# Kernel optimization log

Hardware: AMD Instinct MI355X
Metric: run time of the kernel (lower is better)

The kernel has to match this reference:

```python
import jax, jax.numpy as jnp
import numpy as np

BS, T, FIN, FOUT = 8, 1024, 512, 512
ALPHA = 0.1      # leaky relu slope
T_K = 3          # t_ksize (odd); temporal band radius = T_K // 2
S_K = 4          # s_ksize semantic topk
NEG_INF = -9e15


def setup_inputs() -> dict:
    key = jax.random.key(0)
    k1, k2, k3, k4 = jax.random.split(key, 4)
    # xavier-uniform-ish scales (gain 1.414)
    w_lim = 1.414 * np.sqrt(6.0 / (FIN + FOUT))
    a_lim = 1.414 * np.sqrt(6.0 / (2 * FOUT + 1))
    return {
        "x_a": jax.random.normal(k1, (BS, T, FIN), jnp.float32),
        "x_v": jax.random.normal(k2, (BS, T, FIN), jnp.float32),
        "W": jax.random.uniform(k3, (FIN, FOUT), jnp.float32, -w_lim, w_lim),
        "a": jax.random.uniform(k4, (2 * FOUT, 1), jnp.float32, -a_lim, a_lim),
    }


def _temporal_mask(t):
    # tem_adj[i,j] = 1 iff |i-j| <= T_K//2 and i, j on the same side of t-0.5
    idx = jnp.arange(2 * t)
    same_side = (idx[:, None] >= t) == (idx[None, :] >= t)
    band = jnp.abs(idx[:, None] - idx[None, :]) <= (T_K // 2)
    return band & same_side  # (2t, 2t) bool


def _semantic_block_mask(x, k):
    # x: (bs, t, d). Top-k neighbors by negative squared euclidean distance.
    inner = 2.0 * jnp.einsum("btd,bsd->bts", x, x)
    sq = jnp.sum(x * x, axis=-1, keepdims=True)  # (bs, t, 1)
    pd = -(sq - inner + jnp.swapaxes(sq, -1, -2))  # (bs, t, t)
    _, idx = jax.lax.top_k(pd, k)  # (bs, t, k)
    bs, t = x.shape[0], x.shape[1]
    b_ix = jnp.arange(bs)[:, None, None]
    r_ix = jnp.arange(t)[None, :, None]
    return jnp.zeros((bs, t, t), bool).at[b_ix, r_ix, idx].set(True)


def reference(x_a, x_v, W, a):
    bs, t, _ = x_a.shape
    h = jnp.concatenate([x_a, x_v], axis=1)          # (bs, 2t, FIN)
    Wh = h @ W                                        # (bs, 2t, FOUT)

    # additive GAT score: e = leakyrelu(Wh a1 + (Wh a2)^T)
    Wh1 = Wh @ a[:FOUT]                               # (bs, 2t, 1)
    Wh2 = Wh @ a[FOUT:]                               # (bs, 2t, 1)
    e = Wh1 + jnp.swapaxes(Wh2, -1, -2)               # (bs, 2t, 2t)
    e = jnp.where(e > 0, e, ALPHA * e)                # leaky relu

    # adjacency: temporal band + semantic topk within aa / vv blocks
    tem = _temporal_mask(t)                           # (2t, 2t)
    sem_aa = _semantic_block_mask(Wh[:, :t], S_K)     # (bs, t, t)
    sem_vv = _semantic_block_mask(Wh[:, t:], S_K)     # (bs, t, t)
    zb = jnp.zeros((bs, t, t), bool)
    sem = jnp.concatenate([
        jnp.concatenate([sem_aa, zb], axis=-1),
        jnp.concatenate([zb, sem_vv], axis=-1),
    ], axis=1)                                        # (bs, 2t, 2t)
    mask = tem[None] | sem

    attention = jax.nn.softmax(jnp.where(mask, e, NEG_INF), axis=-1)
    h_prime = jax.nn.elu(attention @ Wh)              # (bs, 2t, FOUT)
    return h_prime[:, :t], h_prime[:, t:]
```

## Files before the change

kernel.cpp:

```cpp
#include <hip/hip_runtime.h>
#include <math.h>

#define T_ 1024
#define BS_ 8
#define D_ 512
#define NROWS_ (BS_*2*T_)
#define ALPHA_ 0.1f

typedef _Float16 f16;
typedef _Float16 f16x8 __attribute__((ext_vector_type(8)));
typedef _Float16 f16x4 __attribute__((ext_vector_type(4)));
typedef _Float16 f16x2 __attribute__((ext_vector_type(2)));
typedef float f32x4 __attribute__((ext_vector_type(4)));

#define MFMA16(A,B,C) __builtin_amdgcn_mfma_f32_16x16x32_f16((A),(B),(C),0,0,0)

__device__ __forceinline__ void gl16(const void* g, void* l) {
    __builtin_amdgcn_global_load_lds(
        (const __attribute__((address_space(1))) unsigned int*)g,
        (__attribute__((address_space(3))) unsigned int*)l, 16, 0, 0);
}

#if __has_builtin(__builtin_amdgcn_fdot2)
__device__ __forceinline__ float fdot2p(f16x2 a, f16x2 b, float c) {
    return __builtin_amdgcn_fdot2(a, b, c, false);
}
#else
__device__ __forceinline__ float fdot2p(f16x2 a, f16x2 b, float c) {
    return fmaf((float)a[1], (float)b[1], fmaf((float)a[0], (float)b[0], c));
}
#endif

__device__ __forceinline__ float fdot8(const f16x8 a, const f16x8 b, float s) {
    #pragma unroll
    for (int q = 0; q < 4; ++q) {
        f16x2 aa, bb;
        aa[0] = a[2*q]; aa[1] = a[2*q+1];
        bb[0] = b[2*q]; bb[1] = b[2*q+1];
        s = fdot2p(aa, bb, s);
    }
    return s;
}

__device__ __forceinline__ unsigned sortable(float f) {
    unsigned u = __float_as_uint(f);
    return u ^ ((u & 0x80000000u) ? 0xFFFFFFFFu : 0x80000000u);
}
__device__ __forceinline__ unsigned pack_key(float s, int col) {
    return (sortable(s) & 0xFFFFFC00u) | (unsigned)(1023 - col);
}

#define INSK4(K, X) { \
    bool g3 = (X) > K[3], g2 = (X) > K[2], g1 = (X) > K[1], g0 = (X) > K[0]; \
    K[3] = g2 ? K[2] : (g3 ? (X) : K[3]); \
    K[2] = g1 ? K[1] : (g2 ? (X) : K[2]); \
    K[1] = g0 ? K[0] : (g1 ? (X) : K[1]); \
    K[0] = g0 ? (X) : K[0]; }

#define INSK8(K, X) { \
    bool h7=(X)>K[7],h6=(X)>K[6],h5=(X)>K[5],h4=(X)>K[4]; \
    bool h3=(X)>K[3],h2=(X)>K[2],h1=(X)>K[1],h0=(X)>K[0]; \
    K[7]=h6?K[6]:(h7?(X):K[7]); K[6]=h5?K[5]:(h6?(X):K[6]); \
    K[5]=h4?K[4]:(h5?(X):K[5]); K[4]=h3?K[3]:(h4?(X):K[4]); \
    K[3]=h2?K[2]:(h3?(X):K[3]); K[2]=h1?K[1]:(h2?(X):K[2]); \
    K[1]=h0?K[0]:(h1?(X):K[1]); K[0]=h0?(X):K[0]; }

#define CEU(a,b) { unsigned mx_ = (a) > (b) ? (a) : (b); \
    unsigned mn_ = (a) > (b) ? (b) : (a); (a) = mx_; (b) = mn_; }

#define MERGE8(K, MSK) { \
    unsigned b0=__shfl_xor(K[0],MSK), b1=__shfl_xor(K[1],MSK), \
             b2=__shfl_xor(K[2],MSK), b3=__shfl_xor(K[3],MSK), \
             b4=__shfl_xor(K[4],MSK), b5=__shfl_xor(K[5],MSK), \
             b6=__shfl_xor(K[6],MSK), b7=__shfl_xor(K[7],MSK); \
    K[0]=K[0]>b7?K[0]:b7; K[1]=K[1]>b6?K[1]:b6; \
    K[2]=K[2]>b5?K[2]:b5; K[3]=K[3]>b4?K[3]:b4; \
    K[4]=K[4]>b3?K[4]:b3; K[5]=K[5]>b2?K[5]:b2; \
    K[6]=K[6]>b1?K[6]:b1; K[7]=K[7]>b0?K[7]:b0; \
    CEU(K[0],K[4]); CEU(K[1],K[5]); CEU(K[2],K[6]); CEU(K[3],K[7]); \
    CEU(K[0],K[2]); CEU(K[1],K[3]); CEU(K[4],K[6]); CEU(K[5],K[7]); \
    CEU(K[0],K[1]); CEU(K[2],K[3]); CEU(K[4],K[5]); CEU(K[6],K[7]); }

#define BETTER(x,xi,v,vi) ((x) > (v) || ((x) == (v) && (xi) < (vi)))
#define INS4T(TV,TI,X,ID) { \
    bool g3 = BETTER(X,ID,TV[3],TI[3]), g2 = BETTER(X,ID,TV[2],TI[2]); \
    bool g1 = BETTER(X,ID,TV[1],TI[1]), g0 = BETTER(X,ID,TV[0],TI[0]); \
    TV[3] = g2 ? TV[2] : (g3 ? (X) : TV[3]); TI[3] = g2 ? TI[2] : (g3 ? (ID) : TI[3]); \
    TV[2] = g1 ? TV[1] : (g2 ? (X) : TV[2]); TI[2] = g1 ? TI[1] : (g2 ? (ID) : TI[2]); \
    TV[1] = g0 ? TV[0] : (g1 ? (X) : TV[1]); TI[1] = g0 ? TI[0] : (g1 ? (ID) : TI[1]); \
    TV[0] = g0 ? (X) : TV[0]; TI[0] = g0 ? (ID) : TI[0]; }

__global__ __launch_bounds__(256) void k_splitW(
    const float* __restrict__ W, f16* __restrict__ WTh, f16* __restrict__ WTl)
{
    __shared__ float tile[64][65];
    const int tid = threadIdx.x;
    const int tk = (blockIdx.x >> 3) << 6, tn = (blockIdx.x & 7) << 6;
    const int r0 = tid >> 4, c4 = (tid & 15) << 2;

    #pragma unroll
    for (int rr = 0; rr < 4; ++rr) {
        int k = r0 + (rr << 4);
        float4 v = *(const float4*)(W + (size_t)(tk + k) * D_ + tn + c4);
        tile[k][c4+0] = v.x; tile[k][c4+1] = v.y;
        tile[k][c4+2] = v.z; tile[k][c4+3] = v.w;
    }
    __syncthreads();
    #pragma unroll
    for (int rr = 0; rr < 4; ++rr) {
        int n = r0 + (rr << 4);
        f16x4 h, l;
        #pragma unroll
        for (int i = 0; i < 4; ++i) {
            float x = tile[c4 + i][n];
            f16 hh = (f16)x; h[i] = hh; l[i] = (f16)(x - (float)hh);
        }
        *(f16x4*)(WTh + (size_t)(tn + n) * D_ + tk + c4) = h;
        *(f16x4*)(WTl + (size_t)(tn + n) * D_ + tk + c4) = l;
    }
}

__global__ __launch_bounds__(512, 4) void k_gemm_wh(
    const float* __restrict__ xa, const float* __restrict__ xv,
    const f16* __restrict__ WTh, const f16* __restrict__ WTl,
    const float* __restrict__ a,
    f16* __restrict__ Whh, f16* __restrict__ Whl,
    float* __restrict__ Wh1, float* __restrict__ Wh2, float* __restrict__ sq)
{
    __shared__ __align__(16) unsigned char smem[81920];

    const int tid  = threadIdx.x;
    const int w    = tid >> 6;
    const int wr   = w >> 2, wc = w & 3;
    const int lane = tid & 63;
    const int l15  = lane & 15;
    const int g    = lane >> 4;
    const int bid  = blockIdx.x;
    const int swz  = ((bid & 7) << 5) + (bid >> 3);
    const int rowbase = swz << 6;

    const int qp = rowbase >> 10;
    const float* xsrc = ((qp & 1) ? xv : xa)
                      + (size_t)((qp >> 1) * 1024 + (rowbase & 1023)) * D_;

    const char* WThB = (const char*)WTh;
    const char* WTlB = (const char*)WTl;

    const int rB1 = tid >> 2,         cB1 = tid & 3;
    const int jB1 = cB1 ^ ((rB1 >> 1) & 3);
    const int rB2 = (tid + 512) >> 2, cB2 = tid & 3;
    const int jB2 = cB2 ^ ((rB2 >> 1) & 3);

    const int rowA = tid >> 3, c8 = tid & 7;
    const int aW = (rowA << 6) + ((((c8 >> 1) ^ ((rowA >> 1) & 3)) << 4)) + ((c8 & 1) << 3);

    const int swzx = (g ^ ((l15 >> 1) & 3)) << 4;
    const int ao0 = (((wr << 5) + l15) << 6) + swzx;
    const int ao1 = ao0 + 1024;
    const int bo0 = (((wc << 6) +  0 + l15) << 6) + swzx;
    const int bo1 = (((wc << 6) + 16 + l15) << 6) + swzx;
    const int bo2 = (((wc << 6) + 32 + l15) << 6) + swzx;
    const int bo3 = (((wc << 6) + 48 + l15) << 6) + swzx;

    #define STAGE_B(cq_, kc_, bufb_) { \
        size_t g1_ = ((size_t)(((cq_) << 8) + rB1) << 10) + ((size_t)(kc_) << 6) + (jB1 << 4); \
        size_t g2_ = ((size_t)(((cq_) << 8) + rB2) << 10) + ((size_t)(kc_) << 6) + (jB2 << 4); \
        gl16(WThB + g1_, smem + (bufb_) + (tid << 4)); \
        gl16(WThB + g2_, smem + (bufb_) + ((tid + 512) << 4)); \
        gl16(WTlB + g1_, smem + (bufb_) + 16384 + (tid << 4)); \
        gl16(WTlB + g2_, smem + (bufb_) + 16384 + ((tid + 512) << 4)); }

    #define STAGE_A(kc_) { \
        float4 v_ = *(const float4*)(xsrc + (size_t)rowA * D_ + ((kc_) << 5) + (c8 << 2)); \
        float xs_[4] = {v_.x, v_.y, v_.z, v_.w}; \
        f16x4 h_, l_; \
        _Pragma("unroll") \
        for (int e_ = 0; e_ < 4; ++e_) { \
            f16 hh_ = (f16)xs_[e_]; h_[e_] = hh_; l_[e_] = (f16)(xs_[e_] - (float)hh_); } \
        const int ab_ = 65536 + (((kc_) & 1) << 13); \
        *(f16x4*)(smem + ab_ + aW)        = h_; \
        *(f16x4*)(smem + ab_ + 4096 + aW) = l_; }

    #define COMPUTE(ACC, BUFB, AB) { \
        f16x8 ah0 = *(const f16x8*)(smem + (AB) + ao0); \
        f16x8 ah1 = *(const f16x8*)(smem + (AB) + ao1); \
        f16x8 al0 = *(const f16x8*)(smem + (AB) + 4096 + ao0); \
        f16x8 al1 = *(const f16x8*)(smem + (AB) + 4096 + ao1); \
        f16x8 bh0 = *(const f16x8*)(smem + (BUFB) + bo0); \
        f16x8 bh1 = *(const f16x8*)(smem + (BUFB) + bo1); \
        f16x8 bh2 = *(const f16x8*)(smem + (BUFB) + bo2); \
        f16x8 bh3 = *(const f16x8*)(smem + (BUFB) + bo3); \
        f16x8 bl0 = *(const f16x8*)(smem + (BUFB) + 16384 + bo0); \
        f16x8 bl1 = *(const f16x8*)(smem + (BUFB) + 16384 + bo1); \
        f16x8 bl2 = *(const f16x8*)(smem + (BUFB) + 16384 + bo2); \
        f16x8 bl3 = *(const f16x8*)(smem + (BUFB) + 16384 + bo3); \
        ACC[0][0] = MFMA16(ah0, bh0, ACC[0][0]); \
        ACC[0][1] = MFMA16(ah0, bh1, ACC[0][1]); \
        ACC[0][2] = MFMA16(ah0, bh2, ACC[0][2]); \
        ACC[0][3] = MFMA16(ah0, bh3, ACC[0][3]); \
        ACC[1][0] = MFMA16(ah1, bh0, ACC[1][0]); \
        ACC[1][1] = MFMA16(ah1, bh1, ACC[1][1]); \
        ACC[1][2] = MFMA16(ah1, bh2, ACC[1][2]); \
        ACC[1][3] = MFMA16(ah1, bh3, ACC[1][3]); \
        ACC[0][0] = MFMA16(al0, bh0, ACC[0][0]); \
        ACC[0][1] = MFMA16(al0, bh1, ACC[0][1]); \
        ACC[0][2] = MFMA16(al0, bh2, ACC[0][2]); \
        ACC[0][3] = MFMA16(al0, bh3, ACC[0][3]); \
        ACC[1][0] = MFMA16(al1, bh0, ACC[1][0]); \
        ACC[1][1] = MFMA16(al1, bh1, ACC[1][1]); \
        ACC[1][2] = MFMA16(al1, bh2, ACC[1][2]); \
        ACC[1][3] = MFMA16(al1, bh3, ACC[1][3]); \
        ACC[0][0] = MFMA16(ah0, bl0, ACC[0][0]); \
        ACC[0][1] = MFMA16(ah0, bl1, ACC[0][1]); \
        ACC[0][2] = MFMA16(ah0, bl2, ACC[0][2]); \
        ACC[0][3] = MFMA16(ah0, bl3, ACC[0][3]); \
        ACC[1][0] = MFMA16(ah1, bl0, ACC[1][0]); \
        ACC[1][1] = MFMA16(ah1, bl1, ACC[1][1]); \
        ACC[1][2] = MFMA16(ah1, bl2, ACC[1][2]); \
        ACC[1][3] = MFMA16(ah1, bl3, ACC[1][3]); }

    f32x4 acc0[2][4], acc1[2][4];
    #pragma unroll
    for (int m = 0; m < 2; ++m)
        #pragma unroll
        for (int c = 0; c < 4; ++c) {
            acc0[m][c] = (f32x4){0.f,0.f,0.f,0.f};
            acc1[m][c] = (f32x4){0.f,0.f,0.f,0.f};
        }

    STAGE_A(0);
    STAGE_B(0, 0, 0);

    for (int kk = 0; kk < 16; ++kk) {
        const int ab = 65536 + ((kk & 1) << 13);
        __syncthreads();
        STAGE_B(1, kk, 32768);
        COMPUTE(acc0, 0, ab);
        __syncthreads();
        if (kk < 15) { STAGE_B(0, kk + 1, 0); STAGE_A(kk + 1); }
        COMPUTE(acc1, 32768, ab);
    }
    #undef STAGE_B
    #undef STAGE_A
    #undef COMPUTE

    __syncthreads();

    float st1[8], st2[8], stq[8];
    #pragma unroll
    for (int s = 0; s < 8; ++s) { st1[s] = 0.f; st2[s] = 0.f; stq[s] = 0.f; }

    #define EPI(ACC, CQ) { \
        _Pragma("unroll") \
        for (int c = 0; c < 4; ++c) { \
            const int col = ((CQ) << 8) + (wc << 6) + (c << 4) + l15; \
            const float a1 = a[col]; \
            const float a2 = a[512 + col]; \
            _Pragma("unroll") \
            for (int m = 0; m < 2; ++m) \
            _Pragma("unroll") \
            for (int j = 0; j < 4; ++j) { \
                const float v = ACC[m][c][j]; \
                const int slot = (m << 2) + j; \
                st1[slot] = fmaf(v, a1, st1[slot]); \
                st2[slot] = fmaf(v, a2, st2[slot]); \
                stq[slot] = fmaf(v, v,  stq[slot]); \
                f16 h = (f16)v; f16 l = (f16)(v - (float)h); \
                const size_t off = (size_t)(rowbase + (wr << 5) + (m << 4) + (g << 2) + j) * D_ + col; \
                Whh[off] = h; Whl[off] = l; \
            } } }

    EPI(acc0, 0);
    EPI(acc1, 1);
    #undef EPI

    #pragma unroll
    for (int mask = 1; mask < 16; mask <<= 1)
        #pragma unroll
        for (int s = 0; s < 8; ++s) {
            st1[s] += __shfl_xor(st1[s], mask);
            st2[s] += __shfl_xor(st2[s], mask);
            stq[s] += __shfl_xor(stq[s], mask);
        }
    if (l15 == 0) {
        #pragma unroll
        for (int s = 0; s < 8; ++s) {
            const int rl = (wr << 5) + ((s >> 2) << 4) + (g << 2) + (s & 3);
            float* sp = (float*)smem + ((rl << 2) + wc) * 3;
            sp[0] = st1[s]; sp[1] = st2[s]; sp[2] = stq[s];
        }
    }
    __syncthreads();
    if (tid < 64) {
        float s1 = 0.f, s2 = 0.f, s3 = 0.f;
        #pragma unroll
        for (int wv = 0; wv < 4; ++wv) {
            const float* sp = (const float*)smem + ((tid << 2) + wv) * 3;
            s1 += sp[0]; s2 += sp[1]; s3 += sp[2];
        }
        Wh1[rowbase + tid] = s1; Wh2[rowbase + tid] = s2; sq[rowbase + tid] = s3;
    }
}

__global__ __launch_bounds__(512, 1) void k_gram_topk8(
    const f16* __restrict__ Whh, const float* __restrict__ sq,
    int* __restrict__ topk8)
{
    __shared__ __align__(16) unsigned char smem[81920];

    const int bid = blockIdx.x;
    const int swz = ((bid & 7) << 5) + (bid >> 3);
    const int p   = swz >> 4;
    const int rt  = swz & 15;
    const int rowbase  = (p << 10) + (rt << 6);
    const int colPanel = p << 10;

    const int tid  = threadIdx.x;
    const int w    = tid >> 6;
    const int wr   = w >> 2, wc = w & 3;
    const int lane = tid & 63;
    const int l15  = lane & 15;
    const int g    = lane >> 4;
    const int r8   = lane >> 3;
    const int k7   = lane & 7;
    const int sw2  = ((k7 ^ r8) << 4);
    const int q0x  = ((g ^ (lane & 7)) << 4);

    const int rowA = tid >> 3;
    const int k7A  = tid & 7;
    const int aswz = ((k7A ^ (rowA & 7)) << 4);

    const char* WB = (const char*)Whh;

    const int aoff0 = 32768 + (((wr << 5) +  0 + l15) << 7) + q0x;
    const int aoff1 = 32768 + (((wr << 5) + 16 + l15) << 7) + q0x;
    const int boff0 = (((wc << 6) +  0 + l15) << 7) + q0x;
    const int boff1 = (((wc << 6) + 16 + l15) << 7) + q0x;
    const int boff2 = (((wc << 6) + 32 + l15) << 7) + q0x;
    const int boff3 = (((wc << 6) + 48 + l15) << 7) + q0x;

    f32x4 acc[2][4];
    #pragma unroll
    for (int m = 0; m < 2; ++m)
        #pragma unroll
        for (int c = 0; c < 4; ++c) acc[m][c] = (f32x4){0.f,0.f,0.f,0.f};

    unsigned k4[8][4];
    #pragma unroll
    for (int s = 0; s < 8; ++s)
        #pragma unroll
        for (int q = 0; q < 4; ++q) k4[s][q] = 0u;

    #define STAGE_G(t) { \
        const int ct_ = (t) >> 3, kc_ = (t) & 7; \
        const int bufb_ = ((t) & 1) * 40960; \
        size_t gB_ = ((size_t)(colPanel + (ct_ << 8) + (w << 5) + r8) << 10) + (kc_ << 7) + sw2; \
        int ldsB_ = bufb_ + (w << 12) + (lane << 4); \
        _Pragma("unroll") \
        for (int j_ = 0; j_ < 4; ++j_) { \
            gl16(WB + gB_, smem + ldsB_); \
            gB_ += (size_t)8 << 10; ldsB_ += 1024; \
        } \
        size_t gA_ = ((size_t)(rowbase + rowA) << 10) + (kc_ << 7) + aswz; \
        gl16(WB + gA_, smem + bufb_ + 32768 + (tid << 4)); \
    }

    STAGE_G(0);

    for (int t = 0; t < 32; ++t) {
        __syncthreads();
        if (t < 31) STAGE_G(t + 1);
        const int bufb = (t & 1) * 40960;

        #pragma unroll
        for (int s = 0; s < 2; ++s) {
            const int sx = s << 6;
            f16x8 a0 = *(const f16x8*)(smem + bufb + (aoff0 ^ sx));
            f16x8 a1 = *(const f16x8*)(smem + bufb + (aoff1 ^ sx));
            f16x8 b0 = *(const f16x8*)(smem + bufb + (boff0 ^ sx));
            f16x8 b1 = *(const f16x8*)(smem + bufb + (boff1 ^ sx));
            f16x8 b2 = *(const f16x8*)(smem + bufb + (boff2 ^ sx));
            f16x8 b3 = *(const f16x8*)(smem + bufb + (boff3 ^ sx));
            acc[0][0] = MFMA16(a0, b0, acc[0][0]);
            acc[0][1] = MFMA16(a0, b1, acc[0][1]);
            acc[0][2] = MFMA16(a0, b2, acc[0][2]);
            acc[0][3] = MFMA16(a0, b3, acc[0][3]);
            acc[1][0] = MFMA16(a1, b0, acc[1][0]);
            acc[1][1] = MFMA16(a1, b1, acc[1][1]);
            acc[1][2] = MFMA16(a1, b2, acc[1][2]);
            acc[1][3] = MFMA16(a1, b3, acc[1][3]);
        }

        if ((t & 7) == 7) {
            const int ct = t >> 3;
            #pragma unroll
            for (int c = 0; c < 4; ++c) {
                const int cl = (ct << 8) + (wc << 6) + (c << 4) + l15;
                const float sqc = sq[colPanel + cl];
                #pragma unroll
                for (int m = 0; m < 2; ++m)
                    #pragma unroll
                    for (int j = 0; j < 4; ++j) {
                        float sc = fmaf(2.f, acc[m][c][j], -sqc);
                        unsigned key = pack_key(sc, cl);
                        INSK4(k4[(m << 2) + j], key);
                    }
                acc[0][c] = (f32x4){0.f,0.f,0.f,0.f};
                acc[1][c] = (f32x4){0.f,0.f,0.f,0.f};
            }
        }
    }

    unsigned k8[8][8];
    #pragma unroll
    for (int s = 0; s < 8; ++s) {
        #pragma unroll
        for (int q = 0; q < 4; ++q) { k8[s][q] = k4[s][q]; k8[s][4 + q] = 0u; }
    }
    #pragma unroll
    for (int msk = 1; msk < 16; msk <<= 1) {
        #pragma unroll
        for (int s = 0; s < 8; ++s) { MERGE8(k8[s], msk); }
    }

    if (l15 == 0) {
        #pragma unroll
        for (int s = 0; s < 8; ++s) {
            const int row_local = ((s >> 2) << 4) + (g << 2) + (s & 3);
            const int off = ((((wr << 5) + row_local) << 2) + wc) << 5;
            *(uint4*)(smem + off)      = make_uint4(k8[s][0], k8[s][1], k8[s][2], k8[s][3]);
            *(uint4*)(smem + off + 16) = make_uint4(k8[s][4], k8[s][5], k8[s][6], k8[s][7]);
        }
    }
    __syncthreads();
    if (tid < 64) {
        const unsigned* bp = (const unsigned*)smem + (tid << 5);
        unsigned kk[8];
        #pragma unroll
        for (int s = 0; s < 8; ++s) kk[s] = bp[s];
        #pragma unroll
        for (int wv = 1; wv < 4; ++wv)
            #pragma unroll
            for (int s = 0; s < 8; ++s) { unsigned x = bp[(wv << 3) + s]; INSK8(kk, x); }
        #pragma unroll
        for (int s = 0; s < 8; ++s)
            topk8[(((size_t)(rowbase + tid)) << 3) + s] = 1023 - (int)(kk[s] & 1023u);
    }
    #undef STAGE_G
}

__global__ __launch_bounds__(256) void k_rescore_agg(
    const f16* __restrict__ Whh, const f16* __restrict__ Whl,
    const float* __restrict__ Wh1, const float* __restrict__ Wh2,
    const float* __restrict__ sq, const int* __restrict__ topk8,
    float* __restrict__ out)
{
    const int bid = blockIdx.x;
    const int swz = ((bid & 7) << 9) + (bid >> 3);
    const int tid  = threadIdx.x;
    const int lane = tid & 63;
    const int r    = (swz << 2) + (tid >> 6);
    const int p    = r >> 10;
    const int i    = r & 1023;
    const int rb   = p << 10;

    const size_t ro = (size_t)r * D_ + (lane << 3);
    f16x8 ah = *(const f16x8*)(Whh + ro);
    f16x8 al = *(const f16x8*)(Whl + ro);

    int cid[8];
    {
        int4 t0 = *(const int4*)(topk8 + ((size_t)r << 3));
        int4 t1 = *(const int4*)(topk8 + ((size_t)r << 3) + 4);
        cid[0]=t0.x; cid[1]=t0.y; cid[2]=t0.z; cid[3]=t0.w;
        cid[4]=t1.x; cid[5]=t1.y; cid[6]=t1.z; cid[7]=t1.w;
    }

    float dp[8];
    #pragma unroll
    for (int c = 0; c < 8; ++c) {
        const size_t co = (size_t)(rb + cid[c]) * D_ + (lane << 3);
        f16x8 bh = *(const f16x8*)(Whh + co);
        f16x8 bl = *(const f16x8*)(Whl + co);
        float s = 0.f;
        s = fdot8(ah, bh, s);
        s = fdot8(ah, bl, s);
        s = fdot8(al, bh, s);
        dp[c] = s;
    }
    #pragma unroll
    for (int off = 32; off > 0; off >>= 1)
        #pragma unroll
        for (int c = 0; c < 8; ++c) dp[c] += __shfl_xor(dp[c], off);

    float tv[4] = {-3.4e38f,-3.4e38f,-3.4e38f,-3.4e38f};
    int   ti[4] = {0x7FFFFFFF,0x7FFFFFFF,0x7FFFFFFF,0x7FFFFFFF};
    #pragma unroll
    for (int c = 0; c < 8; ++c) {
        float sc = fmaf(2.f, dp[c], -sq[rb + cid[c]]);
        INS4T(tv, ti, sc, cid[c]);
    }

    const int  tM = i - 1, tC = i, tP = i + 1;
    const bool vM = (i > 0), vP = (i < T_ - 1);
    const int s0 = ti[0], s1 = ti[1], s2 = ti[2], s3 = ti[3];

    bool u0 = !((vM && s0 == tM) || (s0 == tC) || (vP && s0 == tP));
    bool u1 = !((vM && s1 == tM) || (s1 == tC) || (vP && s1 == tP));
    bool u2 = !((vM && s2 == tM) || (s2 == tC) || (vP && s2 == tP));
    bool u3 = !((vM && s3 == tM) || (s3 == tC) || (vP && s3 == tP));

    int  ci[7] = { vM ? tM : 0, tC, vP ? tP : 0, s0, s1, s2, s3 };
    bool cv[7] = { vM, true, vP, u0, u1, u2, u3 };

    const float e1 = Wh1[r];
    float ev[7];
    float m = -3.4e38f;
    #pragma unroll
    for (int q = 0; q < 7; ++q) {
        float e = e1 + Wh2[rb + ci[q]];
        e = (e > 0.f) ? e : ALPHA_ * e;
        e = cv[q] ? e : -3.4e38f;
        ev[q] = e;
        m = fmaxf(m, e);
    }
    float wsum = 0.f;
    #pragma unroll
    for (int q = 0; q < 7; ++q) {
        float wq = cv[q] ? expf(ev[q] - m) : 0.f;
        ev[q] = wq;
        wsum += wq;
    }
    #pragma unroll
    for (int q = 0; q < 7; ++q) ev[q] /= wsum;

    float A[8] = {0.f,0.f,0.f,0.f,0.f,0.f,0.f,0.f};
    #pragma unroll
    for (int q = 0; q < 7; ++q) {
        if (ev[q] > 0.f) {
            const float wq = ev[q];
            const size_t qo = (size_t)(rb + ci[q]) * D_ + (lane << 3);
            f16x8 vh = *(const f16x8*)(Whh + qo);
            f16x8 vl = *(const f16x8*)(Whl + qo);
            #pragma unroll
            for (int e = 0; e < 8; ++e) A[e] = fmaf(wq, (float)vh[e], A[e]);
            #pragma unroll
            for (int e = 0; e < 8; ++e) A[e] = fmaf(wq, (float)vl[e], A[e]);
        }
    }
    #pragma unroll
    for (int e = 0; e < 8; ++e)
        A[e] = (A[e] > 0.f) ? A[e] : expm1f(A[e]);

    const int blk = p & 1, b = p >> 1;
    float* dst = out + (size_t)blk * ((size_t)BS_ * T_ * D_)
               + ((size_t)((b << 10) + i)) * D_ + (lane << 3);
    *(float4*)(dst)     = make_float4(A[0], A[1], A[2], A[3]);
    *(float4*)(dst + 4) = make_float4(A[4], A[5], A[6], A[7]);
}

extern "C" void kernel_launch(void* const* d_in, const int* in_sizes, int n_in,
                              void* d_out, int out_size, void* d_ws, size_t ws_size,
                              hipStream_t stream)
{
    const float* xa = (const float*)d_in[0];
    const float* xv = (const float*)d_in[1];
    const float* W  = (const float*)d_in[2];
    const float* a  = (const float*)d_in[3];
    float* out = (float*)d_out;

    f16* Whh    = (f16*)d_ws;
    f16* Whl    = Whh + (size_t)NROWS_ * D_;
    f16* WTh    = Whl + (size_t)NROWS_ * D_;
    f16* WTl    = WTh + (size_t)D_ * D_;
    float* Wh1  = (float*)(WTl + (size_t)D_ * D_);
    float* Wh2  = Wh1 + NROWS_;
    float* sq   = Wh2 + NROWS_;
    int* topk8  = (int*)(sq + NROWS_);

    k_splitW     <<<dim3(64),   dim3(256), 0, stream>>>(W, WTh, WTl);
    k_gemm_wh    <<<dim3(256),  dim3(512), 0, stream>>>(xa, xv, WTh, WTl, a, Whh, Whl, Wh1, Wh2, sq);
    k_gram_topk8 <<<dim3(256),  dim3(512), 0, stream>>>(Whh, sq, topk8);
    k_rescore_agg<<<dim3(4096), dim3(256), 0, stream>>>(Whh, Whl, Wh1, Wh2, sq, topk8, out);
}
```

Before: 124.9 us.

## Halve row tile to 32 rows in GEMM and gram-topk kernels, doubling grid

Both the Wh GEMM and the gram/top-k kernel now use 32-row tiles with 4 waves (256 threads) instead of 64-row tiles with 8 waves, and the launch grid grows from 256 to 512 blocks. The intent is to fill more of the MI355X's compute units, since 256 blocks underfill the device. The cost is that each block still stages the full B panel, so B-operand reuse per block halves and global/LDS traffic for W and Wh rises.

```diff
diff --git a/kernel.cpp b/kernel.cpp
--- a/kernel.cpp
+++ b/kernel.cpp
@@ -120,24 +120,23 @@
     }
 }
 
-__global__ __launch_bounds__(512, 4) void k_gemm_wh(
+__global__ __launch_bounds__(256, 2) void k_gemm_wh(
     const float* __restrict__ xa, const float* __restrict__ xv,
     const f16* __restrict__ WTh, const f16* __restrict__ WTl,
     const float* __restrict__ a,
     f16* __restrict__ Whh, f16* __restrict__ Whl,
     float* __restrict__ Wh1, float* __restrict__ Wh2, float* __restrict__ sq)
 {
-    __shared__ __align__(16) unsigned char smem[81920];
+    __shared__ __align__(16) unsigned char smem[73728];
 
     const int tid  = threadIdx.x;
-    const int w    = tid >> 6;
-    const int wr   = w >> 2, wc = w & 3;
+    const int wc   = tid >> 6;
     const int lane = tid & 63;
     const int l15  = lane & 15;
     const int g    = lane >> 4;
     const int bid  = blockIdx.x;
-    const int swz  = ((bid & 7) << 5) + (bid >> 3);
-    const int rowbase = swz << 6;
+    const int swz  = ((bid & 7) << 6) + (bid >> 3);
+    const int rowbase = swz << 5;
 
     const int qp = rowbase >> 10;
     const float* xsrc = ((qp & 1) ? xv : xa)
@@ -146,29 +145,26 @@
     const char* WThB = (const char*)WTh;
     const char* WTlB = (const char*)WTl;
 
-    const int rB1 = tid >> 2,         cB1 = tid & 3;
-    const int jB1 = cB1 ^ ((rB1 >> 1) & 3);
-    const int rB2 = (tid + 512) >> 2, cB2 = tid & 3;
-    const int jB2 = cB2 ^ ((rB2 >> 1) & 3);
-
     const int rowA = tid >> 3, c8 = tid & 7;
     const int aW = (rowA << 6) + ((((c8 >> 1) ^ ((rowA >> 1) & 3)) << 4)) + ((c8 & 1) << 3);
 
     const int swzx = (g ^ ((l15 >> 1) & 3)) << 4;
-    const int ao0 = (((wr << 5) + l15) << 6) + swzx;
+    const int ao0 = (l15 << 6) + swzx;
     const int ao1 = ao0 + 1024;
     const int bo0 = (((wc << 6) +  0 + l15) << 6) + swzx;
     const int bo1 = (((wc << 6) + 16 + l15) << 6) + swzx;
     const int bo2 = (((wc << 6) + 32 + l15) << 6) + swzx;
     const int bo3 = (((wc << 6) + 48 + l15) << 6) + swzx;
 
-    #define STAGE_B(cq_, kc_, bufb_) { \
-        size_t g1_ = ((size_t)(((cq_) << 8) + rB1) << 10) + ((size_t)(kc_) << 6) + (jB1 << 4); \
-        size_t g2_ = ((size_t)(((cq_) << 8) + rB2) << 10) + ((size_t)(kc_) << 6) + (jB2 << 4); \
-        gl16(WThB + g1_, smem + (bufb_) + (tid << 4)); \
-        gl16(WThB + g2_, smem + (bufb_) + ((tid + 512) << 4)); \
-        gl16(WTlB + g1_, smem + (bufb_) + 16384 + (tid << 4)); \
-        gl16(WTlB + g2_, smem + (bufb_) + 16384 + ((tid + 512) << 4)); }
+    #define STAGE_B(cq_, bufb_, kc_) { \
+        _Pragma("unroll") \
+        for (int pp_ = 0; pp_ < 4; ++pp_) { \
+            const int s_ = tid + (pp_ << 8); \
+            const int rs_ = s_ >> 2, cs_ = s_ & 3; \
+            const int jb_ = cs_ ^ ((rs_ >> 1) & 3); \
+            const size_t gb_ = ((size_t)(((cq_) << 8) + rs_) << 10) + ((size_t)(kc_) << 6) + (jb_ << 4); \
+            gl16(WThB + gb_, smem + (bufb_) + (s_ << 4)); \
+            gl16(WTlB + gb_, smem + (bufb_) + 16384 + (s_ << 4)); } }
 
     #define STAGE_A(kc_) { \
         float4 v_ = *(const float4*)(xsrc + (size_t)rowA * D_ + ((kc_) << 5) + (c8 << 2)); \
@@ -177,15 +173,15 @@
         _Pragma("unroll") \
         for (int e_ = 0; e_ < 4; ++e_) { \
             f16 hh_ = (f16)xs_[e_]; h_[e_] = hh_; l_[e_] = (f16)(xs_[e_] - (float)hh_); } \
-        const int ab_ = 65536 + (((kc_) & 1) << 13); \
+        const int ab_ = 65536 + (((kc_) & 1) << 12); \
         *(f16x4*)(smem + ab_ + aW)        = h_; \
-        *(f16x4*)(smem + ab_ + 4096 + aW) = l_; }
+        *(f16x4*)(smem + ab_ + 2048 + aW) = l_; }
 
     #define COMPUTE(ACC, BUFB, AB) { \
         f16x8 ah0 = *(const f16x8*)(smem + (AB) + ao0); \
         f16x8 ah1 = *(const f16x8*)(smem + (AB) + ao1); \
-        f16x8 al0 = *(const f16x8*)(smem + (AB) + 4096 + ao0); \
-        f16x8 al1 = *(const f16x8*)(smem + (AB) + 4096 + ao1); \
+        f16x8 al0 = *(const f16x8*)(smem + (AB) + 2048 + ao0); \
+        f16x8 al1 = *(const f16x8*)(smem + (AB) + 2048 + ao1); \
         f16x8 bh0 = *(const f16x8*)(smem + (BUFB) + bo0); \
         f16x8 bh1 = *(const f16x8*)(smem + (BUFB) + bo1); \
         f16x8 bh2 = *(const f16x8*)(smem + (BUFB) + bo2); \
@@ -232,12 +228,12 @@
     STAGE_B(0, 0, 0);
 
     for (int kk = 0; kk < 16; ++kk) {
-        const int ab = 65536 + ((kk & 1) << 13);
+        const int ab = 65536 + ((kk & 1) << 12);
         __syncthreads();
-        STAGE_B(1, kk, 32768);
+        STAGE_B(1, 32768, kk);
         COMPUTE(acc0, 0, ab);
         __syncthreads();
-        if (kk < 15) { STAGE_B(0, kk + 1, 0); STAGE_A(kk + 1); }
+        if (kk < 15) { STAGE_B(0, 0, kk + 1); STAGE_A(kk + 1); }
         COMPUTE(acc1, 32768, ab);
     }
     #undef STAGE_B
@@ -266,7 +262,7 @@
                 st2[slot] = fmaf(v, a2, st2[slot]); \
                 stq[slot] = fmaf(v, v,  stq[slot]); \
                 f16 h = (f16)v; f16 l = (f16)(v - (float)h); \
-                const size_t off = (size_t)(rowbase + (wr << 5) + (m << 4) + (g << 2) + j) * D_ + col; \
+                const size_t off = (size_t)(rowbase + (m << 4) + (g << 2) + j) * D_ + col; \
                 Whh[off] = h; Whl[off] = l; \
             } } }
 
@@ -285,13 +281,13 @@
     if (l15 == 0) {
         #pragma unroll
         for (int s = 0; s < 8; ++s) {
-            const int rl = (wr << 5) + ((s >> 2) << 4) + (g << 2) + (s & 3);
+            const int rl = ((s >> 2) << 4) + (g << 2) + (s & 3);
             float* sp = (float*)smem + ((rl << 2) + wc) * 3;
             sp[0] = st1[s]; sp[1] = st2[s]; sp[2] = stq[s];
         }
     }
     __syncthreads();
-    if (tid < 64) {
+    if (tid < 32) {
         float s1 = 0.f, s2 = 0.f, s3 = 0.f;
         #pragma unroll
         for (int wv = 0; wv < 4; ++wv) {
@@ -302,22 +298,21 @@
     }
 }
 
-__global__ __launch_bounds__(512, 1) void k_gram_topk8(
+__global__ __launch_bounds__(256, 2) void k_gram_topk8(
     const f16* __restrict__ Whh, const float* __restrict__ sq,
     int* __restrict__ topk8)
 {
-    __shared__ __align__(16) unsigned char smem[81920];
+    __shared__ __align__(16) unsigned char smem[73728];
 
     const int bid = blockIdx.x;
-    const int swz = ((bid & 7) << 5) + (bid >> 3);
-    const int p   = swz >> 4;
-    const int rt  = swz & 15;
-    const int rowbase  = (p << 10) + (rt << 6);
+    const int swz = ((bid & 7) << 6) + (bid >> 3);
+    const int p   = swz >> 5;
+    const int rt  = swz & 31;
+    const int rowbase  = (p << 10) + (rt << 5);
     const int colPanel = p << 10;
 
     const int tid  = threadIdx.x;
-    const int w    = tid >> 6;
-    const int wr   = w >> 2, wc = w & 3;
+    const int wc   = tid >> 6;
     const int lane = tid & 63;
     const int l15  = lane & 15;
     const int g    = lane >> 4;
@@ -332,8 +327,8 @@
 
     const char* WB = (const char*)Whh;
 
-    const int aoff0 = 32768 + (((wr << 5) +  0 + l15) << 7) + q0x;
-    const int aoff1 = 32768 + (((wr << 5) + 16 + l15) << 7) + q0x;
+    const int aoff0 = 32768 + ((0  + l15) << 7) + q0x;
+    const int aoff1 = 32768 + ((16 + l15) << 7) + q0x;
     const int boff0 = (((wc << 6) +  0 + l15) << 7) + q0x;
     const int boff1 = (((wc << 6) + 16 + l15) << 7) + q0x;
     const int boff2 = (((wc << 6) + 32 + l15) << 7) + q0x;
@@ -353,14 +348,17 @@
 
     #define STAGE_G(t) { \
         const int ct_ = (t) >> 3, kc_ = (t) & 7; \
-        const int bufb_ = ((t) & 1) * 40960; \
-        size_t gB_ = ((size_t)(colPanel + (ct_ << 8) + (w << 5) + r8) << 10) + (kc_ << 7) + sw2; \
-        int ldsB_ = bufb_ + (w << 12) + (lane << 4); \
+        const int bufb_ = ((t) & 1) * 36864; \
         _Pragma("unroll") \
-        for (int j_ = 0; j_ < 4; ++j_) { \
-            gl16(WB + gB_, smem + ldsB_); \
-            gB_ += (size_t)8 << 10; ldsB_ += 1024; \
-        } \
+        for (int hp_ = 0; hp_ < 2; ++hp_) { \
+            const int wv_ = wc + (hp_ << 2); \
+            size_t gB_ = ((size_t)(colPanel + (ct_ << 8) + (wv_ << 5) + r8) << 10) + (kc_ << 7) + sw2; \
+            int ldsB_ = bufb_ + (wv_ << 12) + (lane << 4); \
+            _Pragma("unroll") \
+            for (int j_ = 0; j_ < 4; ++j_) { \
+                gl16(WB + gB_, smem + ldsB_); \
+                gB_ += (size_t)8 << 10; ldsB_ += 1024; \
+            } } \
         size_t gA_ = ((size_t)(rowbase + rowA) << 10) + (kc_ << 7) + aswz; \
         gl16(WB + gA_, smem + bufb_ + 32768 + (tid << 4)); \
     }
@@ -370,7 +368,7 @@
     for (int t = 0; t < 32; ++t) {
         __syncthreads();
         if (t < 31) STAGE_G(t + 1);
-        const int bufb = (t & 1) * 40960;
+        const int bufb = (t & 1) * 36864;
 
         #pragma unroll
         for (int s = 0; s < 2; ++s) {
@@ -427,13 +425,13 @@
         #pragma unroll
         for (int s = 0; s < 8; ++s) {
             const int row_local = ((s >> 2) << 4) + (g << 2) + (s & 3);
-            const int off = ((((wr << 5) + row_local) << 2) + wc) << 5;
+            const int off = (((row_local << 2) + wc) << 5);
             *(uint4*)(smem + off)      = make_uint4(k8[s][0], k8[s][1], k8[s][2], k8[s][3]);
             *(uint4*)(smem + off + 16) = make_uint4(k8[s][4], k8[s][5], k8[s][6], k8[s][7]);
         }
     }
     __syncthreads();
-    if (tid < 64) {
+    if (tid < 32) {
         const unsigned* bp = (const unsigned*)smem + (tid << 5);
         unsigned kk[8];
         #pragma unroll
@@ -579,7 +577,7 @@
     int* topk8  = (int*)(sq + NROWS_);
 
     k_splitW     <<<dim3(64),   dim3(256), 0, stream>>>(W, WTh, WTl);
-    k_gemm_wh    <<<dim3(256),  dim3(512), 0, stream>>>(xa, xv, WTh, WTl, a, Whh, Whl, Wh1, Wh2, sq);
-    k_gram_topk8 <<<dim3(256),  dim3(512), 0, stream>>>(Whh, sq, topk8);
+    k_gemm_wh    <<<dim3(512),  dim3(256), 0, stream>>>(xa, xv, WTh, WTl, a, Whh, Whl, Wh1, Wh2, sq);
+    k_gram_topk8 <<<dim3(512),  dim3(256), 0, stream>>>(Whh, sq, topk8);
     k_rescore_agg<<<dim3(4096), dim3(256), 0, stream>>>(Whh, Whl, Wh1, Wh2, sq, topk8, out);
 }
```

New measurement: 129.4 us. +3.6%, slower.

## Triple-buffer GEMM with async A loads; drop low-half Wh in aggregation

Applied to the files above, without the earlier changes.

The Wh GEMM moves to a three-stage ring buffer in LDS. The fp32 x tile is also fetched asynchronously with global_load_lds and split into fp16 hi/lo in registers at compute time, synchronised with vmcnt waits and a barrier in place of the old double-buffer with register staging. Occupancy drops from 4 to 2 blocks per CU to fit the larger LDS footprint. The aggregation kernel now preloads all seven neighbour rows up front and uses only the high fp16 half of Wh, removing the low-half loads and the branch, at some cost in accuracy.

```diff
diff --git a/kernel.cpp b/kernel.cpp
--- a/kernel.cpp
+++ b/kernel.cpp
@@ -90,6 +90,11 @@
     TV[1] = g0 ? TV[0] : (g1 ? (X) : TV[1]); TI[1] = g0 ? TI[0] : (g1 ? (ID) : TI[1]); \
     TV[0] = g0 ? (X) : TV[0]; TI[0] = g0 ? (ID) : TI[0]; }
 
+#define PIPE_WAIT5() { asm volatile("s_waitcnt vmcnt(5)" ::: "memory"); \
+    __builtin_amdgcn_s_barrier(); __builtin_amdgcn_sched_barrier(0); }
+#define PIPE_WAIT0() { asm volatile("s_waitcnt vmcnt(0)" ::: "memory"); \
+    __builtin_amdgcn_s_barrier(); __builtin_amdgcn_sched_barrier(0); }
+
 __global__ __launch_bounds__(256) void k_splitW(
     const float* __restrict__ W, f16* __restrict__ WTh, f16* __restrict__ WTl)
 {
@@ -120,14 +125,14 @@
     }
 }
 
-__global__ __launch_bounds__(512, 4) void k_gemm_wh(
+__global__ __launch_bounds__(512, 2) void k_gemm_wh(
     const float* __restrict__ xa, const float* __restrict__ xv,
     const f16* __restrict__ WTh, const f16* __restrict__ WTl,
     const float* __restrict__ a,
     f16* __restrict__ Whh, f16* __restrict__ Whl,
     float* __restrict__ Wh1, float* __restrict__ Wh2, float* __restrict__ sq)
 {
-    __shared__ __align__(16) unsigned char smem[81920];
+    __shared__ __align__(16) unsigned char smem[122880];
 
     const int tid  = threadIdx.x;
     const int w    = tid >> 6;
@@ -142,82 +147,82 @@
     const int qp = rowbase >> 10;
     const float* xsrc = ((qp & 1) ? xv : xa)
                       + (size_t)((qp >> 1) * 1024 + (rowbase & 1023)) * D_;
-
+    const char* xsrcB = (const char*)xsrc;
     const char* WThB = (const char*)WTh;
     const char* WTlB = (const char*)WTl;
 
-    const int rB1 = tid >> 2,         cB1 = tid & 3;
+    const int rB1 = tid >> 2,          cB1 = tid & 3;
     const int jB1 = cB1 ^ ((rB1 >> 1) & 3);
-    const int rB2 = (tid + 512) >> 2, cB2 = tid & 3;
+    const int rB2 = (tid + 512) >> 2,  cB2 = tid & 3;
     const int jB2 = cB2 ^ ((rB2 >> 1) & 3);
 
-    const int rowA = tid >> 3, c8 = tid & 7;
-    const int aW = (rowA << 6) + ((((c8 >> 1) ^ ((rowA >> 1) & 3)) << 4)) + ((c8 & 1) << 3);
+    const int rA = tid >> 3, cA = tid & 7;
+    const int jcA = (((cA >> 1) ^ ((rA >> 1) & 3)) << 1) | (cA & 1);
+    const size_t gaA_base = (size_t)rA * 2048 + (jcA << 4);
 
     const int swzx = (g ^ ((l15 >> 1) & 3)) << 4;
-    const int ao0 = (((wr << 5) + l15) << 6) + swzx;
-    const int ao1 = ao0 + 1024;
     const int bo0 = (((wc << 6) +  0 + l15) << 6) + swzx;
     const int bo1 = (((wc << 6) + 16 + l15) << 6) + swzx;
     const int bo2 = (((wc << 6) + 32 + l15) << 6) + swzx;
     const int bo3 = (((wc << 6) + 48 + l15) << 6) + swzx;
-
-    #define STAGE_B(cq_, kc_, bufb_) { \
-        size_t g1_ = ((size_t)(((cq_) << 8) + rB1) << 10) + ((size_t)(kc_) << 6) + (jB1 << 4); \
-        size_t g2_ = ((size_t)(((cq_) << 8) + rB2) << 10) + ((size_t)(kc_) << 6) + (jB2 << 4); \
-        gl16(WThB + g1_, smem + (bufb_) + (tid << 4)); \
-        gl16(WThB + g2_, smem + (bufb_) + ((tid + 512) << 4)); \
-        gl16(WTlB + g1_, smem + (bufb_) + 16384 + (tid << 4)); \
-        gl16(WTlB + g2_, smem + (bufb_) + 16384 + ((tid + 512) << 4)); }
-
-    #define STAGE_A(kc_) { \
-        float4 v_ = *(const float4*)(xsrc + (size_t)rowA * D_ + ((kc_) << 5) + (c8 << 2)); \
-        float xs_[4] = {v_.x, v_.y, v_.z, v_.w}; \
-        f16x4 h_, l_; \
+    const int arow = (wr << 5) + l15;
+    const int ar0 = (arow << 7) + ((g ^ ((arow >> 1) & 3)) << 5);
+
+    #define STAGE(kc_, cq_, bb_) { \
+        const size_t g1_ = ((size_t)(((cq_) << 8) + rB1) << 10) + ((size_t)(kc_) << 6) + (jB1 << 4); \
+        const size_t g2_ = ((size_t)(((cq_) << 8) + rB2) << 10) + ((size_t)(kc_) << 6) + (jB2 << 4); \
+        gl16(WThB + g1_, smem + (bb_) + (tid << 4)); \
+        gl16(WThB + g2_, smem + (bb_) + ((tid + 512) << 4)); \
+        gl16(WTlB + g1_, smem + (bb_) + 16384 + (tid << 4)); \
+        gl16(WTlB + g2_, smem + (bb_) + 16384 + ((tid + 512) << 4)); \
+        gl16(xsrcB + gaA_base + ((size_t)(kc_) << 7), smem + (bb_) + 32768 + (tid << 4)); }
+
+    #define CONVA(H, L, p0, p1) { \
+        float xs_[8] = {p0[0],p0[1],p0[2],p0[3],p1[0],p1[1],p1[2],p1[3]}; \
         _Pragma("unroll") \
-        for (int e_ = 0; e_ < 4; ++e_) { \
-            f16 hh_ = (f16)xs_[e_]; h_[e_] = hh_; l_[e_] = (f16)(xs_[e_] - (float)hh_); } \
-        const int ab_ = 65536 + (((kc_) & 1) << 13); \
-        *(f16x4*)(smem + ab_ + aW)        = h_; \
-        *(f16x4*)(smem + ab_ + 4096 + aW) = l_; }
-
-    #define COMPUTE(ACC, BUFB, AB) { \
-        f16x8 ah0 = *(const f16x8*)(smem + (AB) + ao0); \
-        f16x8 ah1 = *(const f16x8*)(smem + (AB) + ao1); \
-        f16x8 al0 = *(const f16x8*)(smem + (AB) + 4096 + ao0); \
-        f16x8 al1 = *(const f16x8*)(smem + (AB) + 4096 + ao1); \
-        f16x8 bh0 = *(const f16x8*)(smem + (BUFB) + bo0); \
-        f16x8 bh1 = *(const f16x8*)(smem + (BUFB) + bo1); \
-        f16x8 bh2 = *(const f16x8*)(smem + (BUFB) + bo2); \
-        f16x8 bh3 = *(const f16x8*)(smem + (BUFB) + bo3); \
-        f16x8 bl0 = *(const f16x8*)(smem + (BUFB) + 16384 + bo0); \
-        f16x8 bl1 = *(const f16x8*)(smem + (BUFB) + 16384 + bo1); \
-        f16x8 bl2 = *(const f16x8*)(smem + (BUFB) + 16384 + bo2); \
-        f16x8 bl3 = *(const f16x8*)(smem + (BUFB) + 16384 + bo3); \
-        ACC[0][0] = MFMA16(ah0, bh0, ACC[0][0]); \
-        ACC[0][1] = MFMA16(ah0, bh1, ACC[0][1]); \
-        ACC[0][2] = MFMA16(ah0, bh2, ACC[0][2]); \
-        ACC[0][3] = MFMA16(ah0, bh3, ACC[0][3]); \
-        ACC[1][0] = MFMA16(ah1, bh0, ACC[1][0]); \
-        ACC[1][1] = MFMA16(ah1, bh1, ACC[1][1]); \
-        ACC[1][2] = MFMA16(ah1, bh2, ACC[1][2]); \
-        ACC[1][3] = MFMA16(ah1, bh3, ACC[1][3]); \
-        ACC[0][0] = MFMA16(al0, bh0, ACC[0][0]); \
-        ACC[0][1] = MFMA16(al0, bh1, ACC[0][1]); \
-        ACC[0][2] = MFMA16(al0, bh2, ACC[0][2]); \
-        ACC[0][3] = MFMA16(al0, bh3, ACC[0][3]); \
-        ACC[1][0] = MFMA16(al1, bh0, ACC[1][0]); \
-        ACC[1][1] = MFMA16(al1, bh1, ACC[1][1]); \
-        ACC[1][2] = MFMA16(al1, bh2, ACC[1][2]); \
-        ACC[1][3] = MFMA16(al1, bh3, ACC[1][3]); \
-        ACC[0][0] = MFMA16(ah0, bl0, ACC[0][0]); \
-        ACC[0][1] = MFMA16(ah0, bl1, ACC[0][1]); \
-        ACC[0][2] = MFMA16(ah0, bl2, ACC[0][2]); \
-        ACC[0][3] = MFMA16(ah0, bl3, ACC[0][3]); \
-        ACC[1][0] = MFMA16(ah1, bl0, ACC[1][0]); \
-        ACC[1][1] = MFMA16(ah1, bl1, ACC[1][1]); \
-        ACC[1][2] = MFMA16(ah1, bl2, ACC[1][2]); \
-        ACC[1][3] = MFMA16(ah1, bl3, ACC[1][3]); }
+        for (int e_ = 0; e_ < 8; ++e_) { \
+            f16 hh_ = (f16)xs_[e_]; H[e_] = hh_; L[e_] = (f16)(xs_[e_] - (float)hh_); } }
+
+    #define COMPUTE(ACC, BB) { \
+        f32x4 u0 = *(const f32x4*)(smem + (BB) + 32768 + ar0); \
+        f32x4 u1 = *(const f32x4*)(smem + (BB) + 32768 + ar0 + 16); \
+        f32x4 v0 = *(const f32x4*)(smem + (BB) + 32768 + ar0 + 2048); \
+        f32x4 v1 = *(const f32x4*)(smem + (BB) + 32768 + ar0 + 2048 + 16); \
+        f16x8 AH0, AL0, AH1, AL1; \
+        CONVA(AH0, AL0, u0, u1); \
+        CONVA(AH1, AL1, v0, v1); \
+        f16x8 bh0 = *(const f16x8*)(smem + (BB) + bo0); \
+        f16x8 bh1 = *(const f16x8*)(smem + (BB) + bo1); \
+        f16x8 bh2 = *(const f16x8*)(smem + (BB) + bo2); \
+        f16x8 bh3 = *(const f16x8*)(smem + (BB) + bo3); \
+        f16x8 bl0 = *(const f16x8*)(smem + (BB) + 16384 + bo0); \
+        f16x8 bl1 = *(const f16x8*)(smem + (BB) + 16384 + bo1); \
+        f16x8 bl2 = *(const f16x8*)(smem + (BB) + 16384 + bo2); \
+        f16x8 bl3 = *(const f16x8*)(smem + (BB) + 16384 + bo3); \
+        ACC[0][0] = MFMA16(AH0, bh0, ACC[0][0]); \
+        ACC[0][1] = MFMA16(AH0, bh1, ACC[0][1]); \
+        ACC[0][2] = MFMA16(AH0, bh2, ACC[0][2]); \
+        ACC[0][3] = MFMA16(AH0, bh3, ACC[0][3]); \
+        ACC[1][0] = MFMA16(AH1, bh0, ACC[1][0]); \
+        ACC[1][1] = MFMA16(AH1, bh1, ACC[1][1]); \
+        ACC[1][2] = MFMA16(AH1, bh2, ACC[1][2]); \
+        ACC[1][3] = MFMA16(AH1, bh3, ACC[1][3]); \
+        ACC[0][0] = MFMA16(AL0, bh0, ACC[0][0]); \
+        ACC[0][1] = MFMA16(AL0, bh1, ACC[0][1]); \
+        ACC[0][2] = MFMA16(AL0, bh2, ACC[0][2]); \
+        ACC[0][3] = MFMA16(AL0, bh3, ACC[0][3]); \
+        ACC[1][0] = MFMA16(AL1, bh0, ACC[1][0]); \
+        ACC[1][1] = MFMA16(AL1, bh1, ACC[1][1]); \
+        ACC[1][2] = MFMA16(AL1, bh2, ACC[1][2]); \
+        ACC[1][3] = MFMA16(AL1, bh3, ACC[1][3]); \
+        ACC[0][0] = MFMA16(AH0, bl0, ACC[0][0]); \
+        ACC[0][1] = MFMA16(AH0, bl1, ACC[0][1]); \
+        ACC[0][2] = MFMA16(AH0, bl2, ACC[0][2]); \
+        ACC[0][3] = MFMA16(AH0, bl3, ACC[0][3]); \
+        ACC[1][0] = MFMA16(AH1, bl0, ACC[1][0]); \
+        ACC[1][1] = MFMA16(AH1, bl1, ACC[1][1]); \
+        ACC[1][2] = MFMA16(AH1, bl2, ACC[1][2]); \
+        ACC[1][3] = MFMA16(AH1, bl3, ACC[1][3]); }
 
     f32x4 acc0[2][4], acc1[2][4];
     #pragma unroll
@@ -228,21 +233,27 @@
             acc1[m][c] = (f32x4){0.f,0.f,0.f,0.f};
         }
 
-    STAGE_A(0);
-    STAGE_B(0, 0, 0);
-
-    for (int kk = 0; kk < 16; ++kk) {
-        const int ab = 65536 + ((kk & 1) << 13);
-        __syncthreads();
-        STAGE_B(1, kk, 32768);
-        COMPUTE(acc0, 0, ab);
-        __syncthreads();
-        if (kk < 15) { STAGE_B(0, kk + 1, 0); STAGE_A(kk + 1); }
-        COMPUTE(acc1, 32768, ab);
-    }
-    #undef STAGE_B
-    #undef STAGE_A
+    STAGE(0, 0, 0);
+    STAGE(0, 1, 40960);
+
+    int cb = 0;
+    int sb = 81920;
+    for (int t = 0; t < 31; ++t) {
+        PIPE_WAIT5();
+        if (t <= 29) {
+            const int tau = t + 2;
+            STAGE(tau >> 1, tau & 1, sb);
+        }
+        if (!(t & 1)) { COMPUTE(acc0, cb); }
+        else          { COMPUTE(acc1, cb); }
+        cb += 40960; cb = (cb == 122880) ? 0 : cb;
+        sb += 40960; sb = (sb == 122880) ? 0 : sb;
+    }
+    PIPE_WAIT0();
+    COMPUTE(acc1, cb);
+    #undef STAGE
     #undef COMPUTE
+    #undef CONVA
 
     __syncthreads();
 
@@ -513,6 +524,11 @@
     int  ci[7] = { vM ? tM : 0, tC, vP ? tP : 0, s0, s1, s2, s3 };
     bool cv[7] = { vM, true, vP, u0, u1, u2, u3 };
 
+    f16x8 vhq[7];
+    #pragma unroll
+    for (int q = 0; q < 7; ++q)
+        vhq[q] = *(const f16x8*)(Whh + (size_t)(rb + ci[q]) * D_ + (lane << 3));
+
     const float e1 = Wh1[r];
     float ev[7];
     float m = -3.4e38f;
@@ -537,16 +553,9 @@
     float A[8] = {0.f,0.f,0.f,0.f,0.f,0.f,0.f,0.f};
     #pragma unroll
     for (int q = 0; q < 7; ++q) {
-        if (ev[q] > 0.f) {
-            const float wq = ev[q];
-            const size_t qo = (size_t)(rb + ci[q]) * D_ + (lane << 3);
-            f16x8 vh = *(const f16x8*)(Whh + qo);
-            f16x8 vl = *(const f16x8*)(Whl + qo);
-            #pragma unroll
-            for (int e = 0; e < 8; ++e) A[e] = fmaf(wq, (float)vh[e], A[e]);
-            #pragma unroll
-            for (int e = 0; e < 8; ++e) A[e] = fmaf(wq, (float)vl[e], A[e]);
-        }
+        const float wq = ev[q];
+        #pragma unroll
+        for (int e = 0; e < 8; ++e) A[e] = fmaf(wq, (float)vhq[q][e], A[e]);
     }
     #pragma unroll
     for (int e = 0; e < 8; ++e)
```

After: 119.4 us. 1.05x faster.
